# Kernel optimization log

Measured on AMD Instinct MI355X. Metric: run time of the kernel, lower is better.

Reference implementation:

```python
import jax, jax.numpy as jnp
import numpy as np

TOP_K = 8
NUM_EXPERTS = 256
NUM_GROUPS = 8
TOPK_GROUP = 4
SCALE = 2.5
EPS = 1e-20


def setup_inputs() -> dict:
    key = jax.random.key(0)
    k1, k2, k3 = jax.random.split(key, 3)
    T, H = 8192, 7168
    hidden_states = jax.random.normal(k1, (T, H), dtype=jnp.float32)
    # scale ~ kaiming-ish so logits are O(1) and sigmoid is not saturated
    weight = jax.random.normal(k2, (NUM_EXPERTS, H), dtype=jnp.float32) * (H ** -0.5)
    e_score_correction_bias = jax.random.normal(k3, (NUM_EXPERTS,), dtype=jnp.float32) * 0.1
    return {"hidden_states": hidden_states, "weight": weight,
            "e_score_correction_bias": e_score_correction_bias}


def reference(hidden_states, weight, e_score_correction_bias):
    T = hidden_states.shape[0]
    epg = NUM_EXPERTS // NUM_GROUPS  # experts per group
    # gating logits: [T, E]
    logits = jnp.einsum('th,eh->te', hidden_states.astype(jnp.float32),
                        weight.astype(jnp.float32))
    scores = jax.nn.sigmoid(logits)
    scores_for_choice = scores + e_score_correction_bias[None, :]
    # group score = sum of top-2 corrected scores within each group: [T, G]
    grouped = scores_for_choice.reshape(T, NUM_GROUPS, epg)
    top2, _ = jax.lax.top_k(grouped, 2)
    group_scores = top2.sum(axis=-1)
    # select topk_group groups, build mask [T, G]
    _, group_idx = jax.lax.top_k(group_scores, TOPK_GROUP)
    group_mask = jnp.zeros((T, NUM_GROUPS), dtype=scores.dtype)
    group_mask = group_mask.at[jnp.arange(T)[:, None], group_idx].set(1.0)
    # expand to expert mask [T, E]
    score_mask = jnp.repeat(group_mask, epg, axis=1)
    tmp_scores = jnp.where(score_mask > 0, scores_for_choice, 0.0)
    # top_k experts among allowed groups
    _, topk_idx = jax.lax.top_k(tmp_scores, TOP_K)
    # gather UNcorrected scores as weights
    topk_weight = jnp.take_along_axis(scores, topk_idx, axis=1)
    topk_weight = topk_weight / (topk_weight.sum(axis=-1, keepdims=True) + EPS)
    topk_weight = topk_weight * SCALE
    return topk_idx, topk_weight
```

## Files before the change

### kernel.cpp

```cpp
#include <hip/hip_runtime.h>
#include <cmath>

typedef __attribute__((ext_vector_type(8))) _Float16 half8;
typedef __attribute__((ext_vector_type(8))) unsigned short ushort8;
typedef __attribute__((ext_vector_type(4))) float f32x4;

#define HH 7168
#define NE 256
#define NQ 224
#define NITER 56
#define TOPK 8
#define TOPKG 4
#define WSC 1024.f
#define INV_WS (1.f/1024.f)
#define C1 (1.f/2048.f)
#define C2 (1.f/4194304.f)

__device__ __forceinline__ void split2(float x, unsigned short& h, unsigned short& m){
  const _Float16 hh = (_Float16)x;
  const float r = x - (float)hh;
  const _Float16 mm = (_Float16)(r * 2048.f);
  h = __builtin_bit_cast(unsigned short, hh);
  m = __builtin_bit_cast(unsigned short, mm);
}

__global__ __launch_bounds__(256) void prep_w(const float* __restrict__ wgt,
                                              unsigned short* __restrict__ bh,
                                              unsigned short* __restrict__ bm){
  const int b = blockIdx.x;
  const int nt = b & 15, qb = (b >> 4) * 4;
  const int w = threadIdx.x >> 6, L = threadIdx.x & 63;
  const int q = qb + w;
  const int e = nt*16 + (L & 15);
  const int k0 = 32*q + 8*(L >> 4);
  const float4 a0 = *(const float4*)(wgt + (size_t)e*HH + k0);
  const float4 a1 = *(const float4*)(wgt + (size_t)e*HH + k0 + 4);
  const float v[8] = {a0.x,a0.y,a0.z,a0.w,a1.x,a1.y,a1.z,a1.w};
  ushort8 h8, m8;
#pragma unroll
  for(int j=0;j<8;j++){ unsigned short hh,mm; split2(v[j]*WSC, hh, mm); h8[j]=hh; m8[j]=mm; }
  const size_t base = ((size_t)(q*16+nt)*64 + L)*8;
  *(ushort8*)(bh+base) = h8;
  *(ushort8*)(bm+base) = m8;
}

#define STIDX(buf,lvl,mt,q,row) (((((buf)*2+(lvl))*16 + (mt)*4 + (q))*64 + (row))*8)
__global__ __launch_bounds__(512,2)
void gemm(const float* __restrict__ hs,
          const unsigned short* __restrict__ bhp,
          const unsigned short* __restrict__ bmp,
          float* __restrict__ lgout){
  __shared__ __align__(16) unsigned short alds[32768];

  const int tid = threadIdx.x, lane = tid & 63, w = tid >> 6;
  const int b = blockIdx.x;
  const int slice = (b >> 2) & 1;
  const int tg = (b >> 3)*4 + (b & 3);
  const int tb = tg*64, eb = slice*128;
  const int mtp = w >> 2, ntp = w & 3;

  const half8* __restrict__ bhv = (const half8*)bhp;
  const half8* __restrict__ bmv = (const half8*)bmp;

  f32x4 ksum[2][2], kcmp[2][2];
#pragma unroll
  for(int a=0;a<2;a++)
#pragma unroll
    for(int c=0;c<2;c++){ ksum[a][c]=f32x4{0,0,0,0}; kcmp[a][c]=f32x4{0,0,0,0}; }

  const int tokS = tid >> 3, cS = tid & 7;
  const int mtS = tokS >> 4, m16S = tokS & 15, qS = cS >> 1;
  const int rowA = (cS & 1)*32 + m16S;
  const float* agp = hs + (size_t)(tb + tokS)*HH + cS*16;

  float4 ga[4];
#pragma unroll
  for(int u=0;u<4;u++) ga[u] = *(const float4*)(agp + 4*u);

  auto stage = [&](int buf){
    unsigned short h[16], m[16];
    const float* gv = (const float*)ga;
#pragma unroll
    for(int p=0;p<16;p++) split2(gv[p], h[p], m[p]);
#pragma unroll
    for(int lvl=0; lvl<2; lvl++){
      const unsigned short* src = lvl ? m : h;
      ushort8 lo, hi;
#pragma unroll
      for(int j=0;j<8;j++){ lo[j]=src[j]; hi[j]=src[8+j]; }
      const int ia = STIDX(buf,lvl,mtS,qS,rowA);
      *(ushort8*)&alds[ia]        = lo;
      *(ushort8*)&alds[ia + 128]  = hi;
    }
  };

  stage(0);
  half8 Bh[2], Bm[2];
#pragma unroll
  for(int ntl=0;ntl<2;ntl++){
    const int slot = ((0*16 + slice*8 + ntp*2 + ntl)*64 + lane);
    Bh[ntl] = bhv[slot]; Bm[ntl] = bmv[slot];
  }
  __syncthreads();

  for(int i=0;i<NITER;i++){
    const int cur = i & 1, nb = cur ^ 1;
    if(i+1 < NITER){
      const float* ap = agp + (size_t)(i+1)*128;
#pragma unroll
      for(int u=0;u<4;u++) ga[u] = *(const float4*)(ap + 4*u);
    }
    f32x4 c0[2][2], c1[2][2], c2[2][2];
#pragma unroll
    for(int a=0;a<2;a++)
#pragma unroll
      for(int c=0;c<2;c++){ c0[a][c]=f32x4{0,0,0,0}; c1[a][c]=f32x4{0,0,0,0}; c2[a][c]=f32x4{0,0,0,0}; }

#pragma unroll
    for(int s=0;s<4;s++){
      const int q = i*4 + s;
      half8 ah[2], am[2];
#pragma unroll
      for(int mtl=0;mtl<2;mtl++){
        const int mt = mtp*2 + mtl;
        ah[mtl] = *(const half8*)&alds[STIDX(cur,0,mt,s,lane)];
        am[mtl] = *(const half8*)&alds[STIDX(cur,1,mt,s,lane)];
      }
      half8 BhN[2], BmN[2];
      const bool more = (q+1 < NQ);
      if(more){
#pragma unroll
        for(int ntl=0;ntl<2;ntl++){
          const int slot = (((q+1)*16 + slice*8 + ntp*2 + ntl)*64 + lane);
          BhN[ntl] = bhv[slot]; BmN[ntl] = bmv[slot];
        }
      }
#pragma unroll
      for(int mtl=0;mtl<2;mtl++)
#pragma unroll
        for(int ntl=0;ntl<2;ntl++){
          c0[mtl][ntl] = __builtin_amdgcn_mfma_f32_16x16x32_f16(ah[mtl], Bh[ntl], c0[mtl][ntl], 0,0,0);
          c1[mtl][ntl] = __builtin_amdgcn_mfma_f32_16x16x32_f16(ah[mtl], Bm[ntl], c1[mtl][ntl], 0,0,0);
          c1[mtl][ntl] = __builtin_amdgcn_mfma_f32_16x16x32_f16(am[mtl], Bh[ntl], c1[mtl][ntl], 0,0,0);
          c2[mtl][ntl] = __builtin_amdgcn_mfma_f32_16x16x32_f16(am[mtl], Bm[ntl], c2[mtl][ntl], 0,0,0);
        }
      if(more){
#pragma unroll
        for(int ntl=0;ntl<2;ntl++){ Bh[ntl]=BhN[ntl]; Bm[ntl]=BmN[ntl]; }
      }
    }
    if(i+1 < NITER) stage(nb);
#pragma unroll
    for(int a=0;a<2;a++)
#pragma unroll
      for(int c=0;c<2;c++)
#pragma unroll
        for(int r=0;r<4;r++){
          const float v = c0[a][c][r] + c1[a][c][r]*C1 + c2[a][c][r]*C2;
          const float y = v - kcmp[a][c][r];
          const float t = ksum[a][c][r] + y;
          kcmp[a][c][r] = (t - ksum[a][c][r]) - y;
          ksum[a][c][r] = t;
        }
    __syncthreads();
  }

#pragma unroll
  for(int mtl=0;mtl<2;mtl++)
#pragma unroll
    for(int ntl=0;ntl<2;ntl++)
#pragma unroll
      for(int r=0;r<4;r++){
        const int tok = (mtp*2+mtl)*16 + (lane>>4)*4 + r;
        const int e = (ntp*2+ntl)*16 + (lane&15);
        const float lg = (ksum[mtl][ntl][r] - kcmp[mtl][ntl][r]) * INV_WS;
        lgout[(size_t)(tb+tok)*NE + eb + e] = lg;
      }
}

__global__ __launch_bounds__(256)
void gate(const float* __restrict__ lg, const float* __restrict__ bias,
          float* __restrict__ out, int T){
  const int tid = threadIdx.x, lane = tid & 63, wv = tid >> 6;
  const int tb = blockIdx.x*32;
  const float4 bias4 = *(const float4*)(bias + 4*lane);
  const int g = lane >> 3;
  const float NEG_INF = -__builtin_inff();

  for (int it = 0; it < 8; ++it) {
    const int t = tb + wv*8 + it;
    const float4 l4 = *(const float4*)(lg + (size_t)t*NE + 4*lane);
    float4 r4;
    r4.x = 1.f/(1.f + expf(-l4.x));
    r4.y = 1.f/(1.f + expf(-l4.y));
    r4.z = 1.f/(1.f + expf(-l4.z));
    r4.w = 1.f/(1.f + expf(-l4.w));
    float4 s4;
    s4.x = r4.x + bias4.x; s4.y = r4.y + bias4.y;
    s4.z = r4.z + bias4.z; s4.w = r4.w + bias4.w;

    float m1 = s4.x, m2 = NEG_INF;
    if (s4.y > m1) { m2 = m1; m1 = s4.y; } else if (s4.y > m2) m2 = s4.y;
    if (s4.z > m1) { m2 = m1; m1 = s4.z; } else if (s4.z > m2) m2 = s4.z;
    if (s4.w > m1) { m2 = m1; m1 = s4.w; } else if (s4.w > m2) m2 = s4.w;
#pragma unroll
    for (int m = 1; m <= 4; m <<= 1) {
      const float o1 = __shfl_xor(m1, m);
      const float o2 = __shfl_xor(m2, m);
      const float nm1 = fmaxf(m1, o1);
      const float nm2 = fmaxf(fminf(m1, o1), fmaxf(m2, o2));
      m1 = nm1; m2 = nm2;
    }
    const float gs = m1 + m2;

    float gsv[8];
#pragma unroll
    for (int j = 0; j < 8; ++j) gsv[j] = __shfl(gs, j * 8);

    unsigned gm = 0;
#pragma unroll
    for (int r = 0; r < TOPKG; ++r) {
      float best = NEG_INF; int bj = 0;
#pragma unroll
      for (int j = 0; j < 8; ++j) {
        const bool avail = !((gm >> j) & 1u);
        if (avail && gsv[j] > best) { best = gsv[j]; bj = j; }
      }
      gm |= 1u << bj;
    }
    const bool allowed = (gm >> g) & 1u;

    float v0 = allowed ? s4.x : 0.f;
    float v1 = allowed ? s4.y : 0.f;
    float v2 = allowed ? s4.z : 0.f;
    float v3 = allowed ? s4.w : 0.f;

    float sumw = 0.f;
    int myidx = 0; float myraw = 0.f;
#pragma unroll
    for (int r = 0; r < TOPK; ++r) {
      float bv = v0; int bj = 0;
      if (v1 > bv) { bv = v1; bj = 1; }
      if (v2 > bv) { bv = v2; bj = 2; }
      if (v3 > bv) { bv = v3; bj = 3; }
      int bidx = 4 * lane + bj;
#pragma unroll
      for (int m = 1; m < 64; m <<= 1) {
        const float ov = __shfl_xor(bv, m);
        const int   oi = __shfl_xor(bidx, m);
        if (ov > bv || (ov == bv && oi < bidx)) { bv = ov; bidx = oi; }
      }
      const int oj = bidx & 3;
      const float cand = (oj == 0) ? r4.x
                       : (oj == 1) ? r4.y
                       : (oj == 2) ? r4.z
                       :             r4.w;
      const float raw = __shfl(cand, bidx >> 2);
      sumw += raw;
      if (lane == r) { myidx = bidx; myraw = raw; }
      if (lane == (bidx >> 2)) {
        if      (oj == 0) v0 = NEG_INF;
        else if (oj == 1) v1 = NEG_INF;
        else if (oj == 2) v2 = NEG_INF;
        else              v3 = NEG_INF;
      }
    }

    if (lane < TOPK) {
      out[(size_t)t * TOPK + lane] = (float)myidx;
      out[(size_t)T * TOPK + (size_t)t * TOPK + lane] = myraw / (sumw + 1e-20f) * 2.5f;
    }
  }
}

extern "C" void kernel_launch(void* const* d_in, const int* in_sizes, int n_in,
                              void* d_out, int out_size, void* d_ws, size_t ws_size,
                              hipStream_t stream) {
  const float* hs   = (const float*)d_in[0];
  const float* wgt  = (const float*)d_in[1];
  const float* bias = (const float*)d_in[2];
  float* out = (float*)d_out;

  const int T = in_sizes[0] / HH;

  unsigned short* bh = (unsigned short*)d_ws;
  unsigned short* bm = bh + (size_t)NE*HH;
  float* lgbuf = (float*)(bm + (size_t)NE*HH);

  hipLaunchKernelGGL(prep_w, dim3(896), dim3(256), 0, stream, wgt, bh, bm);
  hipLaunchKernelGGL(gemm,   dim3(256), dim3(512), 0, stream, hs, bh, bm, lgbuf);
  hipLaunchKernelGGL(gate,   dim3(T/32), dim3(256), 0, stream, lgbuf, bias, out, T);
}
```

Before: 497.9 us.

## Halve GEMM token tile to 32, swizzle LDS, double grid, one token per gate wave

The GEMM block tile drops from 64 to 32 tokens, which halves LDS use and per-wave accumulators. The grid doubles to 512 blocks and launch bounds allow 4 blocks per SM, aiming for better CU coverage and occupancy. An XOR swizzle on the LDS byte address targets bank conflicts. The gate kernel now processes one token per wave with T/4 blocks instead of looping over 8 tokens. The cost is that each B fragment loaded from global memory is reused across half as many tokens, doubling B traffic.

Measured after the change: 465.2 us. -6.6%, faster.

```diff
diff --git a/kernel.cpp b/kernel.cpp
--- a/kernel.cpp
+++ b/kernel.cpp
@@ -44,54 +44,51 @@
   *(ushort8*)(bm+base) = m8;
 }
 
-#define STIDX(buf,lvl,mt,q,row) (((((buf)*2+(lvl))*16 + (mt)*4 + (q))*64 + (row))*8)
-__global__ __launch_bounds__(512,2)
+#define ABYTE(buf,lvl,mt,q,row) (((((buf)*2+(lvl))*8 + (mt)*4 + (q))*64 + (row))*16)
+__device__ __forceinline__ int swz(int bo){ return bo ^ (((bo >> 8) & 7) << 4); }
+
+__global__ __launch_bounds__(512,4)
 void gemm(const float* __restrict__ hs,
           const unsigned short* __restrict__ bhp,
           const unsigned short* __restrict__ bmp,
           float* __restrict__ lgout){
-  __shared__ __align__(16) unsigned short alds[32768];
+  __shared__ __align__(16) unsigned short alds[16384];
+  char* const aldsb = (char*)alds;
 
   const int tid = threadIdx.x, lane = tid & 63, w = tid >> 6;
   const int b = blockIdx.x;
   const int slice = (b >> 2) & 1;
   const int tg = (b >> 3)*4 + (b & 3);
-  const int tb = tg*64, eb = slice*128;
+  const int tb = tg*32, eb = slice*128;
   const int mtp = w >> 2, ntp = w & 3;
 
   const half8* __restrict__ bhv = (const half8*)bhp;
   const half8* __restrict__ bmv = (const half8*)bmp;
 
-  f32x4 ksum[2][2], kcmp[2][2];
-#pragma unroll
-  for(int a=0;a<2;a++)
-#pragma unroll
-    for(int c=0;c<2;c++){ ksum[a][c]=f32x4{0,0,0,0}; kcmp[a][c]=f32x4{0,0,0,0}; }
-
-  const int tokS = tid >> 3, cS = tid & 7;
-  const int mtS = tokS >> 4, m16S = tokS & 15, qS = cS >> 1;
-  const int rowA = (cS & 1)*32 + m16S;
-  const float* agp = hs + (size_t)(tb + tokS)*HH + cS*16;
-
-  float4 ga[4];
-#pragma unroll
-  for(int u=0;u<4;u++) ga[u] = *(const float4*)(agp + 4*u);
+  f32x4 ksum[2], kcmp[2];
+#pragma unroll
+  for(int c=0;c<2;c++){ ksum[c]=f32x4{0,0,0,0}; kcmp[c]=f32x4{0,0,0,0}; }
+
+  const int tokS = tid >> 4, kidx = tid & 15;
+  const int mtS = tokS >> 4, m16S = tokS & 15;
+  const int qS = kidx >> 2, kgS = kidx & 3;
+  const int rowS = kgS*16 + m16S;
+  const float* agp = hs + (size_t)(tb + tokS)*HH + kidx*8;
+
+  float4 ga[2];
+  ga[0] = *(const float4*)(agp);
+  ga[1] = *(const float4*)(agp + 4);
 
   auto stage = [&](int buf){
-    unsigned short h[16], m[16];
+    unsigned short h[8], m[8];
     const float* gv = (const float*)ga;
 #pragma unroll
-    for(int p=0;p<16;p++) split2(gv[p], h[p], m[p]);
-#pragma unroll
-    for(int lvl=0; lvl<2; lvl++){
-      const unsigned short* src = lvl ? m : h;
-      ushort8 lo, hi;
-#pragma unroll
-      for(int j=0;j<8;j++){ lo[j]=src[j]; hi[j]=src[8+j]; }
-      const int ia = STIDX(buf,lvl,mtS,qS,rowA);
-      *(ushort8*)&alds[ia]        = lo;
-      *(ushort8*)&alds[ia + 128]  = hi;
-    }
+    for(int p=0;p<8;p++) split2(gv[p], h[p], m[p]);
+    ushort8 h8, m8;
+#pragma unroll
+    for(int j=0;j<8;j++){ h8[j]=h[j]; m8[j]=m[j]; }
+    *(ushort8*)(aldsb + swz(ABYTE(buf,0,mtS,qS,rowS))) = h8;
+    *(ushort8*)(aldsb + swz(ABYTE(buf,1,mtS,qS,rowS))) = m8;
   };
 
   stage(0);
@@ -107,25 +104,18 @@
     const int cur = i & 1, nb = cur ^ 1;
     if(i+1 < NITER){
       const float* ap = agp + (size_t)(i+1)*128;
-#pragma unroll
-      for(int u=0;u<4;u++) ga[u] = *(const float4*)(ap + 4*u);
-    }
-    f32x4 c0[2][2], c1[2][2], c2[2][2];
-#pragma unroll
-    for(int a=0;a<2;a++)
-#pragma unroll
-      for(int c=0;c<2;c++){ c0[a][c]=f32x4{0,0,0,0}; c1[a][c]=f32x4{0,0,0,0}; c2[a][c]=f32x4{0,0,0,0}; }
+      ga[0] = *(const float4*)(ap);
+      ga[1] = *(const float4*)(ap + 4);
+    }
+    f32x4 c0[2], c1[2], c2[2];
+#pragma unroll
+    for(int c=0;c<2;c++){ c0[c]=f32x4{0,0,0,0}; c1[c]=f32x4{0,0,0,0}; c2[c]=f32x4{0,0,0,0}; }
 
 #pragma unroll
     for(int s=0;s<4;s++){
       const int q = i*4 + s;
-      half8 ah[2], am[2];
-#pragma unroll
-      for(int mtl=0;mtl<2;mtl++){
-        const int mt = mtp*2 + mtl;
-        ah[mtl] = *(const half8*)&alds[STIDX(cur,0,mt,s,lane)];
-        am[mtl] = *(const half8*)&alds[STIDX(cur,1,mt,s,lane)];
-      }
+      const half8 ah = *(const half8*)(aldsb + swz(ABYTE(cur,0,mtp,s,lane)));
+      const half8 am = *(const half8*)(aldsb + swz(ABYTE(cur,1,mtp,s,lane)));
       half8 BhN[2], BmN[2];
       const bool more = (q+1 < NQ);
       if(more){
@@ -136,14 +126,12 @@
         }
       }
 #pragma unroll
-      for(int mtl=0;mtl<2;mtl++)
-#pragma unroll
-        for(int ntl=0;ntl<2;ntl++){
-          c0[mtl][ntl] = __builtin_amdgcn_mfma_f32_16x16x32_f16(ah[mtl], Bh[ntl], c0[mtl][ntl], 0,0,0);
-          c1[mtl][ntl] = __builtin_amdgcn_mfma_f32_16x16x32_f16(ah[mtl], Bm[ntl], c1[mtl][ntl], 0,0,0);
-          c1[mtl][ntl] = __builtin_amdgcn_mfma_f32_16x16x32_f16(am[mtl], Bh[ntl], c1[mtl][ntl], 0,0,0);
-          c2[mtl][ntl] = __builtin_amdgcn_mfma_f32_16x16x32_f16(am[mtl], Bm[ntl], c2[mtl][ntl], 0,0,0);
-        }
+      for(int ntl=0;ntl<2;ntl++){
+        c0[ntl] = __builtin_amdgcn_mfma_f32_16x16x32_f16(ah, Bh[ntl], c0[ntl], 0,0,0);
+        c1[ntl] = __builtin_amdgcn_mfma_f32_16x16x32_f16(ah, Bm[ntl], c1[ntl], 0,0,0);
+        c1[ntl] = __builtin_amdgcn_mfma_f32_16x16x32_f16(am, Bh[ntl], c1[ntl], 0,0,0);
+        c2[ntl] = __builtin_amdgcn_mfma_f32_16x16x32_f16(am, Bm[ntl], c2[ntl], 0,0,0);
+      }
       if(more){
 #pragma unroll
         for(int ntl=0;ntl<2;ntl++){ Bh[ntl]=BhN[ntl]; Bm[ntl]=BmN[ntl]; }
@@ -151,125 +139,118 @@
     }
     if(i+1 < NITER) stage(nb);
 #pragma unroll
-    for(int a=0;a<2;a++)
-#pragma unroll
-      for(int c=0;c<2;c++)
-#pragma unroll
-        for(int r=0;r<4;r++){
-          const float v = c0[a][c][r] + c1[a][c][r]*C1 + c2[a][c][r]*C2;
-          const float y = v - kcmp[a][c][r];
-          const float t = ksum[a][c][r] + y;
-          kcmp[a][c][r] = (t - ksum[a][c][r]) - y;
-          ksum[a][c][r] = t;
-        }
+    for(int c=0;c<2;c++)
+#pragma unroll
+      for(int r=0;r<4;r++){
+        const float v = c0[c][r] + c1[c][r]*C1 + c2[c][r]*C2;
+        const float y = v - kcmp[c][r];
+        const float t = ksum[c][r] + y;
+        kcmp[c][r] = (t - ksum[c][r]) - y;
+        ksum[c][r] = t;
+      }
     __syncthreads();
   }
 
 #pragma unroll
-  for(int mtl=0;mtl<2;mtl++)
-#pragma unroll
-    for(int ntl=0;ntl<2;ntl++)
-#pragma unroll
-      for(int r=0;r<4;r++){
-        const int tok = (mtp*2+mtl)*16 + (lane>>4)*4 + r;
-        const int e = (ntp*2+ntl)*16 + (lane&15);
-        const float lg = (ksum[mtl][ntl][r] - kcmp[mtl][ntl][r]) * INV_WS;
-        lgout[(size_t)(tb+tok)*NE + eb + e] = lg;
-      }
+  for(int ntl=0;ntl<2;ntl++)
+#pragma unroll
+    for(int r=0;r<4;r++){
+      const int tok = mtp*16 + (lane>>4)*4 + r;
+      const int e = (ntp*2+ntl)*16 + (lane&15);
+      const float lg = (ksum[ntl][r] - kcmp[ntl][r]) * INV_WS;
+      lgout[(size_t)(tb+tok)*NE + eb + e] = lg;
+    }
 }
 
 __global__ __launch_bounds__(256)
 void gate(const float* __restrict__ lg, const float* __restrict__ bias,
           float* __restrict__ out, int T){
   const int tid = threadIdx.x, lane = tid & 63, wv = tid >> 6;
-  const int tb = blockIdx.x*32;
+  const int t = blockIdx.x*4 + wv;
   const float4 bias4 = *(const float4*)(bias + 4*lane);
   const int g = lane >> 3;
   const float NEG_INF = -__builtin_inff();
 
-  for (int it = 0; it < 8; ++it) {
-    const int t = tb + wv*8 + it;
-    const float4 l4 = *(const float4*)(lg + (size_t)t*NE + 4*lane);
-    float4 r4;
-    r4.x = 1.f/(1.f + expf(-l4.x));
-    r4.y = 1.f/(1.f + expf(-l4.y));
-    r4.z = 1.f/(1.f + expf(-l4.z));
-    r4.w = 1.f/(1.f + expf(-l4.w));
-    float4 s4;
-    s4.x = r4.x + bias4.x; s4.y = r4.y + bias4.y;
-    s4.z = r4.z + bias4.z; s4.w = r4.w + bias4.w;
-
-    float m1 = s4.x, m2 = NEG_INF;
-    if (s4.y > m1) { m2 = m1; m1 = s4.y; } else if (s4.y > m2) m2 = s4.y;
-    if (s4.z > m1) { m2 = m1; m1 = s4.z; } else if (s4.z > m2) m2 = s4.z;
-    if (s4.w > m1) { m2 = m1; m1 = s4.w; } else if (s4.w > m2) m2 = s4.w;
-#pragma unroll
-    for (int m = 1; m <= 4; m <<= 1) {
-      const float o1 = __shfl_xor(m1, m);
-      const float o2 = __shfl_xor(m2, m);
-      const float nm1 = fmaxf(m1, o1);
-      const float nm2 = fmaxf(fminf(m1, o1), fmaxf(m2, o2));
-      m1 = nm1; m2 = nm2;
-    }
-    const float gs = m1 + m2;
-
-    float gsv[8];
-#pragma unroll
-    for (int j = 0; j < 8; ++j) gsv[j] = __shfl(gs, j * 8);
-
-    unsigned gm = 0;
-#pragma unroll
-    for (int r = 0; r < TOPKG; ++r) {
-      float best = NEG_INF; int bj = 0;
-#pragma unroll
-      for (int j = 0; j < 8; ++j) {
-        const bool avail = !((gm >> j) & 1u);
-        if (avail && gsv[j] > best) { best = gsv[j]; bj = j; }
-      }
-      gm |= 1u << bj;
-    }
-    const bool allowed = (gm >> g) & 1u;
-
-    float v0 = allowed ? s4.x : 0.f;
-    float v1 = allowed ? s4.y : 0.f;
-    float v2 = allowed ? s4.z : 0.f;
-    float v3 = allowed ? s4.w : 0.f;
-
-    float sumw = 0.f;
-    int myidx = 0; float myraw = 0.f;
-#pragma unroll
-    for (int r = 0; r < TOPK; ++r) {
-      float bv = v0; int bj = 0;
-      if (v1 > bv) { bv = v1; bj = 1; }
-      if (v2 > bv) { bv = v2; bj = 2; }
-      if (v3 > bv) { bv = v3; bj = 3; }
-      int bidx = 4 * lane + bj;
-#pragma unroll
-      for (int m = 1; m < 64; m <<= 1) {
-        const float ov = __shfl_xor(bv, m);
-        const int   oi = __shfl_xor(bidx, m);
-        if (ov > bv || (ov == bv && oi < bidx)) { bv = ov; bidx = oi; }
-      }
-      const int oj = bidx & 3;
-      const float cand = (oj == 0) ? r4.x
-                       : (oj == 1) ? r4.y
-                       : (oj == 2) ? r4.z
-                       :             r4.w;
-      const float raw = __shfl(cand, bidx >> 2);
-      sumw += raw;
-      if (lane == r) { myidx = bidx; myraw = raw; }
-      if (lane == (bidx >> 2)) {
-        if      (oj == 0) v0 = NEG_INF;
-        else if (oj == 1) v1 = NEG_INF;
-        else if (oj == 2) v2 = NEG_INF;
-        else              v3 = NEG_INF;
-      }
-    }
-
-    if (lane < TOPK) {
-      out[(size_t)t * TOPK + lane] = (float)myidx;
-      out[(size_t)T * TOPK + (size_t)t * TOPK + lane] = myraw / (sumw + 1e-20f) * 2.5f;
-    }
+  const float4 l4 = *(const float4*)(lg + (size_t)t*NE + 4*lane);
+  float4 r4;
+  r4.x = 1.f/(1.f + expf(-l4.x));
+  r4.y = 1.f/(1.f + expf(-l4.y));
+  r4.z = 1.f/(1.f + expf(-l4.z));
+  r4.w = 1.f/(1.f + expf(-l4.w));
+  float4 s4;
+  s4.x = r4.x + bias4.x; s4.y = r4.y + bias4.y;
+  s4.z = r4.z + bias4.z; s4.w = r4.w + bias4.w;
+
+  float m1 = s4.x, m2 = NEG_INF;
+  if (s4.y > m1) { m2 = m1; m1 = s4.y; } else if (s4.y > m2) m2 = s4.y;
+  if (s4.z > m1) { m2 = m1; m1 = s4.z; } else if (s4.z > m2) m2 = s4.z;
+  if (s4.w > m1) { m2 = m1; m1 = s4.w; } else if (s4.w > m2) m2 = s4.w;
+#pragma unroll
+  for (int m = 1; m <= 4; m <<= 1) {
+    const float o1 = __shfl_xor(m1, m);
+    const float o2 = __shfl_xor(m2, m);
+    const float nm1 = fmaxf(m1, o1);
+    const float nm2 = fmaxf(fminf(m1, o1), fmaxf(m2, o2));
+    m1 = nm1; m2 = nm2;
+  }
+  const float gs = m1 + m2;
+
+  float gsv[8];
+#pragma unroll
+  for (int j = 0; j < 8; ++j) gsv[j] = __shfl(gs, j * 8);
+
+  unsigned gm = 0;
+#pragma unroll
+  for (int r = 0; r < TOPKG; ++r) {
+    float best = NEG_INF; int bj = 0;
+#pragma unroll
+    for (int j = 0; j < 8; ++j) {
+      const bool avail = !((gm >> j) & 1u);
+      if (avail && gsv[j] > best) { best = gsv[j]; bj = j; }
+    }
+    gm |= 1u << bj;
+  }
+  const bool allowed = (gm >> g) & 1u;
+
+  float v0 = allowed ? s4.x : 0.f;
+  float v1 = allowed ? s4.y : 0.f;
+  float v2 = allowed ? s4.z : 0.f;
+  float v3 = allowed ? s4.w : 0.f;
+
+  float sumw = 0.f;
+  int myidx = 0; float myraw = 0.f;
+#pragma unroll
+  for (int r = 0; r < TOPK; ++r) {
+    float bv = v0; int bj = 0;
+    if (v1 > bv) { bv = v1; bj = 1; }
+    if (v2 > bv) { bv = v2; bj = 2; }
+    if (v3 > bv) { bv = v3; bj = 3; }
+    int bidx = 4 * lane + bj;
+#pragma unroll
+    for (int m = 1; m < 64; m <<= 1) {
+      const float ov = __shfl_xor(bv, m);
+      const int   oi = __shfl_xor(bidx, m);
+      if (ov > bv || (ov == bv && oi < bidx)) { bv = ov; bidx = oi; }
+    }
+    const int oj = bidx & 3;
+    const float cand = (oj == 0) ? r4.x
+                     : (oj == 1) ? r4.y
+                     : (oj == 2) ? r4.z
+                     :             r4.w;
+    const float raw = __shfl(cand, bidx >> 2);
+    sumw += raw;
+    if (lane == r) { myidx = bidx; myraw = raw; }
+    if (lane == (bidx >> 2)) {
+      if      (oj == 0) v0 = NEG_INF;
+      else if (oj == 1) v1 = NEG_INF;
+      else if (oj == 2) v2 = NEG_INF;
+      else              v3 = NEG_INF;
+    }
+  }
+
+  if (lane < TOPK) {
+    out[(size_t)t * TOPK + lane] = (float)myidx;
+    out[(size_t)T * TOPK + (size_t)t * TOPK + lane] = myraw / (sumw + 1e-20f) * 2.5f;
   }
 }
 
@@ -288,6 +269,6 @@
   float* lgbuf = (float*)(bm + (size_t)NE*HH);
 
   hipLaunchKernelGGL(prep_w, dim3(896), dim3(256), 0, stream, wgt, bh, bm);
-  hipLaunchKernelGGL(gemm,   dim3(256), dim3(512), 0, stream, hs, bh, bm, lgbuf);
-  hipLaunchKernelGGL(gate,   dim3(T/32), dim3(256), 0, stream, lgbuf, bias, out, T);
-}
+  hipLaunchKernelGGL(gemm,   dim3(512), dim3(512), 0, stream, hs, bh, bm, lgbuf);
+  hipLaunchKernelGGL(gate,   dim3(T/4), dim3(256), 0, stream, lgbuf, bias, out, T);
+}
```
